# Kernel tuning notes

Hardware: AMD Instinct MI355X
Metric: run time of the kernel (lower is better)

## Reference

```python
import jax, jax.numpy as jnp
import numpy as np

NUM_NODES = 17185
D = 6
FEATS = NUM_NODES * D  # 103110
BATCH = 256
EPS = 1e-5


def setup_inputs() -> dict:
    key = jax.random.key(0)
    ks = jax.random.split(key, 4)
    data = jax.random.normal(ks[0], (BATCH, FEATS), dtype=jnp.float32)
    w_blocks = jax.random.normal(ks[1], (NUM_NODES, D, D), dtype=jnp.float32) * (1.0 / np.sqrt(D))
    b_blocks = jax.random.normal(ks[2], (NUM_NODES, D), dtype=jnp.float32) * 0.1
    fc_w = jax.random.normal(ks[3], (FEATS,), dtype=jnp.float32) * (1.0 / np.sqrt(FEATS))
    return {
        "data": data,
        "w_blocks": w_blocks,
        "b_blocks": b_blocks,
        "bn_gamma": jnp.ones((FEATS,), jnp.float32),
        "bn_beta": jnp.zeros((FEATS,), jnp.float32),
        "bn_mean": jnp.zeros((FEATS,), jnp.float32),
        "bn_var": jnp.ones((FEATS,), jnp.float32),
        "fc_w": fc_w,
        "fc_b": jnp.zeros((1,), jnp.float32),
        "bnf_gamma": jnp.ones((1,), jnp.float32),
        "bnf_beta": jnp.zeros((1,), jnp.float32),
        "bnf_mean": jnp.zeros((1,), jnp.float32),
        "bnf_var": jnp.ones((1,), jnp.float32),
    }


def reference(data, w_blocks, b_blocks, bn_gamma, bn_beta, bn_mean, bn_var,
              fc_w, fc_b, bnf_gamma, bnf_beta, bnf_mean, bnf_var):
    B = data.shape[0]
    # block-diagonal batched matmul replacing 17185 tiny Linear(6,6) calls
    x = data.reshape(B, NUM_NODES, D)                       # [B, N, 6]
    xo = jnp.einsum("bni,noi->bno", x, w_blocks) + b_blocks  # torch Linear: x @ W^T + b
    xo = xo.reshape(B, FEATS)                               # hstack ordering == reshape
    # relu -> BatchNorm1d (eval: running stats) -> dropout (identity in eval)
    h = jnp.maximum(xo, 0.0)
    h = (h - bn_mean) * jax.lax.rsqrt(bn_var + EPS) * bn_gamma + bn_beta
    # final linear [FEATS -> 1], BN(1), sigmoid
    y = h @ fc_w + fc_b                                     # [B]
    y = y[:, None]                                          # [B, 1]
    y = (y - bnf_mean) * jax.lax.rsqrt(bnf_var + EPS) * bnf_gamma + bnf_beta
    return jax.nn.sigmoid(y)
```

## Files before the change

### kernel.cpp

```cpp
#include <hip/hip_runtime.h>
#include <stdint.h>

#define NUM_NODES 17185
#define DD 6
#define FEATS (NUM_NODES * DD)
#define BATCH 256
#define EPS 1e-5f

#define NC 256
#define BC 16
#define NCHUNK ((NUM_NODES + NC - 1) / NC)


__global__ __launch_bounds__(NC) void main_kernel(
    const float* __restrict__ data, const float* __restrict__ wb, const float* __restrict__ bb,
    const float* __restrict__ gamma, const float* __restrict__ var, const float* __restrict__ fcw,
    const float* __restrict__ beta, const float* __restrict__ mean,
    float* __restrict__ pm, float* __restrict__ pc) {

    const int tid = threadIdx.x;
    const int n = blockIdx.x * NC + tid;
    const bool valid = (n < NUM_NODES);

    float wreg[36], bias[6], a[6];
    #pragma unroll
    for (int k = 0; k < 36; k++) wreg[k] = 0.f;
    #pragma unroll
    for (int k = 0; k < 6; k++) { bias[k] = 0.f; a[k] = 0.f; }

    float cnode = 0.f;

    if (valid) {
        const float4* wp = (const float4*)(wb + (size_t)n * 36);
        #pragma unroll
        for (int k = 0; k < 9; k++) {
            float4 v = wp[k];
            wreg[4*k] = v.x; wreg[4*k+1] = v.y; wreg[4*k+2] = v.z; wreg[4*k+3] = v.w;
        }
        const float2* bp = (const float2*)(bb + (size_t)n * 6);
        #pragma unroll
        for (int k = 0; k < 3; k++) { float2 v = bp[k]; bias[2*k] = v.x; bias[2*k+1] = v.y; }
        const int f0 = n * 6;
        const float2* gp = (const float2*)(gamma + f0);
        const float2* vp = (const float2*)(var + f0);
        const float2* fp = (const float2*)(fcw + f0);
        float fw[6];
        #pragma unroll
        for (int k = 0; k < 3; k++) {
            float2 g = gp[k], v = vp[k], f = fp[k];
            fw[2*k] = f.x; fw[2*k+1] = f.y;
            a[2*k]   = g.x * rsqrtf(v.x + EPS) * f.x;
            a[2*k+1] = g.y * rsqrtf(v.y + EPS) * f.y;
        }
        if (blockIdx.y == 0) {
            const float2* bep = (const float2*)(beta + f0);
            const float2* mp  = (const float2*)(mean + f0);
            #pragma unroll
            for (int k = 0; k < 3; k++) {
                float2 be = bep[k], m = mp[k];
                cnode += be.x * fw[2*k]   - m.x * a[2*k];
                cnode += be.y * fw[2*k+1] - m.y * a[2*k+1];
            }
        }
    }

    const int b0 = blockIdx.y * BC;
    float acc[BC];
    #pragma unroll
    for (int r = 0; r < BC; r++) acc[r] = 0.f;

    if (valid) {
        const float2* xbase = (const float2*)(data + (size_t)b0 * FEATS + (size_t)n * 6);
        #pragma unroll
        for (int r = 0; r < BC; r++) {
            const float2* xp = xbase + (size_t)r * (FEATS / 2);
            float2 u0 = xp[0], u1 = xp[1], u2 = xp[2];
            float x0 = u0.x, x1 = u0.y, x2 = u1.x, x3 = u1.y, x4 = u2.x, x5 = u2.y;
            #pragma unroll
            for (int o = 0; o < 6; o++) {
                float s = bias[o];
                s = fmaf(x0, wreg[o*6+0], s);
                s = fmaf(x1, wreg[o*6+1], s);
                s = fmaf(x2, wreg[o*6+2], s);
                s = fmaf(x3, wreg[o*6+3], s);
                s = fmaf(x4, wreg[o*6+4], s);
                s = fmaf(x5, wreg[o*6+5], s);
                acc[r] = fmaf(fmaxf(s, 0.f), a[o], acc[r]);
            }
        }
    }

    __shared__ float red[4][BC];
    #pragma unroll
    for (int r = 0; r < BC; r++) {
        float v = acc[r];
        #pragma unroll
        for (int off = 32; off; off >>= 1) v += __shfl_down(v, off);
        if ((tid & 63) == 0) red[tid >> 6][r] = v;
    }

    if (blockIdx.y == 0) {
        float v = cnode;
        #pragma unroll
        for (int off = 32; off; off >>= 1) v += __shfl_down(v, off);
        __shared__ float credd[4];
        if ((tid & 63) == 0) credd[tid >> 6] = v;
        __syncthreads();
        if (tid == 0) pc[blockIdx.x] = credd[0] + credd[1] + credd[2] + credd[3];
    } else {
        __syncthreads();
    }

    if (tid < BC) {
        float s = red[0][tid] + red[1][tid] + red[2][tid] + red[3][tid];
        pm[blockIdx.x * 256 + b0 + tid] = s;
    }
}

__global__ __launch_bounds__(256) void final_kernel(
    const float* __restrict__ pm, const float* __restrict__ pc,
    const float* __restrict__ fcb, const float* __restrict__ bnfg,
    const float* __restrict__ bnfb, const float* __restrict__ bnfm,
    const float* __restrict__ bnfv, float* __restrict__ out) {
    const int b = threadIdx.x;

    float c = (b < NCHUNK) ? pc[b] : 0.f;
    #pragma unroll
    for (int off = 32; off; off >>= 1) c += __shfl_down(c, off);
    __shared__ float red[4];
    if ((b & 63) == 0) red[b >> 6] = c;
    __syncthreads();
    const float c_sum = red[0] + red[1] + red[2] + red[3];

    float y = 0.f;
    #pragma unroll 4
    for (int ch = 0; ch < NCHUNK; ch++) y += pm[ch * 256 + b];

    y += c_sum + fcb[0];
    float sc = bnfg[0] * rsqrtf(bnfv[0] + EPS);
    float z = (y - bnfm[0]) * sc + bnfb[0];
    out[b] = 1.f / (1.f + expf(-z));
}

extern "C" void kernel_launch(void* const* d_in, const int* in_sizes, int n_in,
                              void* d_out, int out_size, void* d_ws, size_t ws_size,
                              hipStream_t stream) {
    const float* data  = (const float*)d_in[0];
    const float* wb    = (const float*)d_in[1];
    const float* bb    = (const float*)d_in[2];
    const float* gamma = (const float*)d_in[3];
    const float* beta  = (const float*)d_in[4];
    const float* mean  = (const float*)d_in[5];
    const float* var   = (const float*)d_in[6];
    const float* fcw   = (const float*)d_in[7];
    const float* fcb   = (const float*)d_in[8];
    const float* bnfg  = (const float*)d_in[9];
    const float* bnfb  = (const float*)d_in[10];
    const float* bnfm  = (const float*)d_in[11];
    const float* bnfv  = (const float*)d_in[12];

    float* pm = (float*)d_ws;
    float* pc = pm + NCHUNK * 256;

    dim3 grid(NCHUNK, BATCH / BC);
    main_kernel<<<grid, NC, 0, stream>>>(data, wb, bb, gamma, var, fcw, beta, mean, pm, pc);

    final_kernel<<<1, 256, 0, stream>>>(pm, pc, fcb, bnfg, bnfb, bnfm, bnfv, (float*)d_out);
}
```

Before: 191.4 us.

## Stage data rows through shared memory with coalesced float4 loads and register prefetch

Replaces the per-thread strided float2 loads of each node's six features with cooperative, coalesced float4 loads of two batch rows per step into a shared-memory tile. The next pair of rows is prefetched into registers while the current pair is computed. The goal is better global-memory coalescing and overlap of loads with compute. It adds two barriers per step, extra registers and a 12 KB shared buffer, and shared reads at a 24-byte stride per thread may hit bank conflicts.

Measured after the change: 198.7 us. 1.04x slower.

```diff
diff --git a/kernel.cpp b/kernel.cpp
--- a/kernel.cpp
+++ b/kernel.cpp
@@ -10,6 +10,8 @@
 #define NC 256
 #define BC 16
 #define NCHUNK ((NUM_NODES + NC - 1) / NC)
+#define SEG (NC * DD)
+#define TOTF ((size_t)BATCH * FEATS)
 
 
 __global__ __launch_bounds__(NC) void main_kernel(
@@ -21,6 +23,8 @@
     const int tid = threadIdx.x;
     const int n = blockIdx.x * NC + tid;
     const bool valid = (n < NUM_NODES);
+
+    __shared__ float xs[2 * SEG];
 
     float wreg[36], bias[6], a[6];
     #pragma unroll
@@ -65,29 +69,64 @@
     }
 
     const int b0 = blockIdx.y * BC;
+    const size_t segbase = (size_t)blockIdx.x * SEG;
     float acc[BC];
     #pragma unroll
     for (int r = 0; r < BC; r++) acc[r] = 0.f;
 
-    if (valid) {
-        const float2* xbase = (const float2*)(data + (size_t)b0 * FEATS + (size_t)n * 6);
-        #pragma unroll
-        for (int r = 0; r < BC; r++) {
-            const float2* xp = xbase + (size_t)r * (FEATS / 2);
+    float4 pf[3];
+    {
+        #pragma unroll
+        for (int k = 0; k < 3; k++) {
+            int j = tid + k * NC;
+            int row = (j < 384) ? 0 : 1;
+            int col = j - row * 384;
+            size_t g = (size_t)(b0 + row) * FEATS + segbase + (size_t)col * 4;
+            if (g + 4 <= TOTF) pf[k] = *(const float4*)(data + g);
+            else pf[k] = make_float4(0.f, 0.f, 0.f, 0.f);
+        }
+    }
+
+    #pragma unroll
+    for (int s = 0; s < 8; s++) {
+        #pragma unroll
+        for (int k = 0; k < 3; k++) {
+            int j = tid + k * NC;
+            ((float4*)xs)[j] = pf[k];
+        }
+        __syncthreads();
+
+        if (s < 7) {
+            #pragma unroll
+            for (int k = 0; k < 3; k++) {
+                int j = tid + k * NC;
+                int row = (j < 384) ? 0 : 1;
+                int col = j - row * 384;
+                size_t g = (size_t)(b0 + 2*(s+1) + row) * FEATS + segbase + (size_t)col * 4;
+                if (g + 4 <= TOTF) pf[k] = *(const float4*)(data + g);
+                else pf[k] = make_float4(0.f, 0.f, 0.f, 0.f);
+            }
+        }
+
+        #pragma unroll
+        for (int rr = 0; rr < 2; rr++) {
+            const float2* xp = (const float2*)(xs + rr * SEG + tid * 6);
             float2 u0 = xp[0], u1 = xp[1], u2 = xp[2];
             float x0 = u0.x, x1 = u0.y, x2 = u1.x, x3 = u1.y, x4 = u2.x, x5 = u2.y;
+            const int r = 2*s + rr;
             #pragma unroll
             for (int o = 0; o < 6; o++) {
-                float s = bias[o];
-                s = fmaf(x0, wreg[o*6+0], s);
-                s = fmaf(x1, wreg[o*6+1], s);
-                s = fmaf(x2, wreg[o*6+2], s);
-                s = fmaf(x3, wreg[o*6+3], s);
-                s = fmaf(x4, wreg[o*6+4], s);
-                s = fmaf(x5, wreg[o*6+5], s);
-                acc[r] = fmaf(fmaxf(s, 0.f), a[o], acc[r]);
+                float v = bias[o];
+                v = fmaf(x0, wreg[o*6+0], v);
+                v = fmaf(x1, wreg[o*6+1], v);
+                v = fmaf(x2, wreg[o*6+2], v);
+                v = fmaf(x3, wreg[o*6+3], v);
+                v = fmaf(x4, wreg[o*6+4], v);
+                v = fmaf(x5, wreg[o*6+5], v);
+                acc[r] = fmaf(fmaxf(v, 0.f), a[o], acc[r]);
             }
         }
+        __syncthreads();
     }
 
     __shared__ float red[4][BC];
```

## Process two nodes per thread with 16-byte data loads and smaller batch chunks

Applied to the files above, without the earlier changes.

Each thread now handles two adjacent nodes (72 weights in registers), so its 12 contiguous input floats can be read with three 16-byte vector loads instead of three 8-byte loads. Blocks shrink to 128 threads and the batch chunk per block drops from 16 to 8 rows, which doubles the grid along the batch axis and so doubles how many times the weight blocks are re-read. The tail chunk keeps a guarded scalar path. Register pressure rises considerably, and launch bounds now request 4 blocks per CU.

Measured after the change: 261.9 us. +36.8%, slower.

```diff
diff --git a/kernel.cpp b/kernel.cpp
--- a/kernel.cpp
+++ b/kernel.cpp
@@ -1,5 +1,6 @@
 #include <hip/hip_runtime.h>
 #include <stdint.h>
+#include <string.h>
 
 #define NUM_NODES 17185
 #define DD 6
@@ -7,59 +8,73 @@
 #define BATCH 256
 #define EPS 1e-5f
 
-#define NC 256
-#define BC 16
-#define NCHUNK ((NUM_NODES + NC - 1) / NC)
-
-
-__global__ __launch_bounds__(NC) void main_kernel(
+#define NT 128
+#define NPB 256
+#define BC 8
+#define NCHUNK ((NUM_NODES + NPB - 1) / NPB)
+#define TOTF ((size_t)BATCH * FEATS)
+
+
+__device__ __forceinline__ void load16(float* dst, const float* src) {
+    __builtin_memcpy(dst, src, 16);
+}
+
+__global__ __launch_bounds__(NT, 4) void main_kernel(
     const float* __restrict__ data, const float* __restrict__ wb, const float* __restrict__ bb,
     const float* __restrict__ gamma, const float* __restrict__ var, const float* __restrict__ fcw,
     const float* __restrict__ beta, const float* __restrict__ mean,
     float* __restrict__ pm, float* __restrict__ pc) {
 
     const int tid = threadIdx.x;
-    const int n = blockIdx.x * NC + tid;
-    const bool valid = (n < NUM_NODES);
-
-    float wreg[36], bias[6], a[6];
-    #pragma unroll
-    for (int k = 0; k < 36; k++) wreg[k] = 0.f;
-    #pragma unroll
-    for (int k = 0; k < 6; k++) { bias[k] = 0.f; a[k] = 0.f; }
+    const int bx = blockIdx.x;
+    const int n0 = bx * NPB + 2 * tid;
+    const int n1 = n0 + 1;
+    const bool v0 = (n0 < NUM_NODES);
+    const bool v1 = (n1 < NUM_NODES);
+
+    float w[72], bias[12], aa[12];
+    #pragma unroll
+    for (int k = 0; k < 72; k++) w[k] = 0.f;
+    #pragma unroll
+    for (int k = 0; k < 12; k++) { bias[k] = 0.f; aa[k] = 0.f; }
 
     float cnode = 0.f;
 
-    if (valid) {
-        const float4* wp = (const float4*)(wb + (size_t)n * 36);
-        #pragma unroll
-        for (int k = 0; k < 9; k++) {
-            float4 v = wp[k];
-            wreg[4*k] = v.x; wreg[4*k+1] = v.y; wreg[4*k+2] = v.z; wreg[4*k+3] = v.w;
-        }
-        const float2* bp = (const float2*)(bb + (size_t)n * 6);
-        #pragma unroll
-        for (int k = 0; k < 3; k++) { float2 v = bp[k]; bias[2*k] = v.x; bias[2*k+1] = v.y; }
-        const int f0 = n * 6;
-        const float2* gp = (const float2*)(gamma + f0);
-        const float2* vp = (const float2*)(var + f0);
-        const float2* fp = (const float2*)(fcw + f0);
-        float fw[6];
-        #pragma unroll
-        for (int k = 0; k < 3; k++) {
-            float2 g = gp[k], v = vp[k], f = fp[k];
-            fw[2*k] = f.x; fw[2*k+1] = f.y;
-            a[2*k]   = g.x * rsqrtf(v.x + EPS) * f.x;
-            a[2*k+1] = g.y * rsqrtf(v.y + EPS) * f.y;
-        }
-        if (blockIdx.y == 0) {
-            const float2* bep = (const float2*)(beta + f0);
-            const float2* mp  = (const float2*)(mean + f0);
+    #pragma unroll
+    for (int nn = 0; nn < 2; nn++) {
+        const int n = n0 + nn;
+        if (n < NUM_NODES) {
+            const float4* wp = (const float4*)(wb + (size_t)n * 36);
+            #pragma unroll
+            for (int k = 0; k < 9; k++) {
+                float4 v = wp[k];
+                w[nn*36 + 4*k] = v.x; w[nn*36 + 4*k+1] = v.y;
+                w[nn*36 + 4*k+2] = v.z; w[nn*36 + 4*k+3] = v.w;
+            }
+            const float2* bp = (const float2*)(bb + (size_t)n * 6);
+            #pragma unroll
+            for (int k = 0; k < 3; k++) { float2 v = bp[k]; bias[nn*6 + 2*k] = v.x; bias[nn*6 + 2*k+1] = v.y; }
+            const int f0 = n * 6;
+            const float2* gp = (const float2*)(gamma + f0);
+            const float2* vp = (const float2*)(var + f0);
+            const float2* fp = (const float2*)(fcw + f0);
+            float fw[6];
             #pragma unroll
             for (int k = 0; k < 3; k++) {
-                float2 be = bep[k], m = mp[k];
-                cnode += be.x * fw[2*k]   - m.x * a[2*k];
-                cnode += be.y * fw[2*k+1] - m.y * a[2*k+1];
+                float2 g = gp[k], v = vp[k], f = fp[k];
+                fw[2*k] = f.x; fw[2*k+1] = f.y;
+                aa[nn*6 + 2*k]   = g.x * rsqrtf(v.x + EPS) * f.x;
+                aa[nn*6 + 2*k+1] = g.y * rsqrtf(v.y + EPS) * f.y;
+            }
+            if (blockIdx.y == 0) {
+                const float2* bep = (const float2*)(beta + f0);
+                const float2* mp  = (const float2*)(mean + f0);
+                #pragma unroll
+                for (int k = 0; k < 3; k++) {
+                    float2 be = bep[k], m = mp[k];
+                    cnode += be.x * fw[2*k]   - m.x * aa[nn*6 + 2*k];
+                    cnode += be.y * fw[2*k+1] - m.y * aa[nn*6 + 2*k+1];
+                }
             }
         }
     }
@@ -69,28 +84,59 @@
     #pragma unroll
     for (int r = 0; r < BC; r++) acc[r] = 0.f;
 
-    if (valid) {
-        const float2* xbase = (const float2*)(data + (size_t)b0 * FEATS + (size_t)n * 6);
+    if (bx < NCHUNK - 1) {
+        const float* base = data + (size_t)b0 * FEATS + (size_t)bx * (NPB * DD) + 12 * tid;
         #pragma unroll
         for (int r = 0; r < BC; r++) {
-            const float2* xp = xbase + (size_t)r * (FEATS / 2);
-            float2 u0 = xp[0], u1 = xp[1], u2 = xp[2];
-            float x0 = u0.x, x1 = u0.y, x2 = u1.x, x3 = u1.y, x4 = u2.x, x5 = u2.y;
-            #pragma unroll
-            for (int o = 0; o < 6; o++) {
-                float s = bias[o];
-                s = fmaf(x0, wreg[o*6+0], s);
-                s = fmaf(x1, wreg[o*6+1], s);
-                s = fmaf(x2, wreg[o*6+2], s);
-                s = fmaf(x3, wreg[o*6+3], s);
-                s = fmaf(x4, wreg[o*6+4], s);
-                s = fmaf(x5, wreg[o*6+5], s);
-                acc[r] = fmaf(fmaxf(s, 0.f), a[o], acc[r]);
+            const float* p = base + (size_t)r * FEATS;
+            float x[12];
+            load16(x,     p);
+            load16(x + 4, p + 4);
+            load16(x + 8, p + 8);
+            #pragma unroll
+            for (int nn = 0; nn < 2; nn++) {
+                #pragma unroll
+                for (int o = 0; o < 6; o++) {
+                    float s = bias[nn*6 + o];
+                    #pragma unroll
+                    for (int i = 0; i < 6; i++)
+                        s = fmaf(x[nn*6 + i], w[nn*36 + o*6 + i], s);
+                    acc[r] = fmaf(fmaxf(s, 0.f), aa[nn*6 + o], acc[r]);
+                }
             }
         }
-    }
-
-    __shared__ float red[4][BC];
+    } else {
+        #pragma unroll
+        for (int r = 0; r < BC; r++) {
+            const int b = b0 + r;
+            float x[12];
+            #pragma unroll
+            for (int k = 0; k < 12; k++) x[k] = 0.f;
+            if (v0) {
+                const float2* xp = (const float2*)(data + (size_t)b * FEATS + (size_t)n0 * 6);
+                float2 u0 = xp[0], u1 = xp[1], u2 = xp[2];
+                x[0] = u0.x; x[1] = u0.y; x[2] = u1.x; x[3] = u1.y; x[4] = u2.x; x[5] = u2.y;
+            }
+            if (v1) {
+                const float2* xp = (const float2*)(data + (size_t)b * FEATS + (size_t)n1 * 6);
+                float2 u0 = xp[0], u1 = xp[1], u2 = xp[2];
+                x[6] = u0.x; x[7] = u0.y; x[8] = u1.x; x[9] = u1.y; x[10] = u2.x; x[11] = u2.y;
+            }
+            #pragma unroll
+            for (int nn = 0; nn < 2; nn++) {
+                #pragma unroll
+                for (int o = 0; o < 6; o++) {
+                    float s = bias[nn*6 + o];
+                    #pragma unroll
+                    for (int i = 0; i < 6; i++)
+                        s = fmaf(x[nn*6 + i], w[nn*36 + o*6 + i], s);
+                    acc[r] = fmaf(fmaxf(s, 0.f), aa[nn*6 + o], acc[r]);
+                }
+            }
+        }
+    }
+
+    __shared__ float red[2][BC];
     #pragma unroll
     for (int r = 0; r < BC; r++) {
         float v = acc[r];
@@ -103,17 +149,17 @@
         float v = cnode;
         #pragma unroll
         for (int off = 32; off; off >>= 1) v += __shfl_down(v, off);
-        __shared__ float credd[4];
+        __shared__ float credd[2];
         if ((tid & 63) == 0) credd[tid >> 6] = v;
         __syncthreads();
-        if (tid == 0) pc[blockIdx.x] = credd[0] + credd[1] + credd[2] + credd[3];
+        if (tid == 0) pc[bx] = credd[0] + credd[1];
     } else {
         __syncthreads();
     }
 
     if (tid < BC) {
-        float s = red[0][tid] + red[1][tid] + red[2][tid] + red[3][tid];
-        pm[blockIdx.x * 256 + b0 + tid] = s;
+        float s = red[0][tid] + red[1][tid];
+        pm[bx * 256 + b0 + tid] = s;
     }
 }
 
@@ -133,7 +179,7 @@
     const float c_sum = red[0] + red[1] + red[2] + red[3];
 
     float y = 0.f;
-    #pragma unroll 4
+    #pragma unroll 8
     for (int ch = 0; ch < NCHUNK; ch++) y += pm[ch * 256 + b];
 
     y += c_sum + fcb[0];
@@ -163,7 +209,7 @@
     float* pc = pm + NCHUNK * 256;
 
     dim3 grid(NCHUNK, BATCH / BC);
-    main_kernel<<<grid, NC, 0, stream>>>(data, wb, bb, gamma, var, fcw, beta, mean, pm, pc);
+    main_kernel<<<grid, NT, 0, stream>>>(data, wb, bb, gamma, var, fcw, beta, mean, pm, pc);
 
     final_kernel<<<1, 256, 0, stream>>>(pm, pc, fcb, bnfg, bnfb, bnfm, bnfv, (float*)d_out);
 }
```

## Fuse final reduction via last-block atomic counter; nontemporal double-buffered data loads

Applied to the files above, without the earlier changes.

Removes the separate final_kernel launch: each block increments a global counter after a threadfence, and the last block to finish does the cross-chunk reduction and sigmoid. The per-row data loads become nontemporal 64-bit loads, issued four rows at a time with a double buffer so the next group is in flight while the current one is computed. This cuts a kernel launch and tail gap and should improve memory-level parallelism, but it adds a memset launch, an atomic per block and higher register pressure.

Result: slower. 362.7 us (+89.4%).

```diff
diff --git a/kernel.cpp b/kernel.cpp
--- a/kernel.cpp
+++ b/kernel.cpp
@@ -10,16 +10,28 @@
 #define NC 256
 #define BC 16
 #define NCHUNK ((NUM_NODES + NC - 1) / NC)
-
+#define NBLK (NCHUNK * (BATCH / BC))
+
+
+__device__ __forceinline__ void nt_load2(const float* p, float& lo, float& hi) {
+    uint64_t u = __builtin_nontemporal_load((const uint64_t*)p);
+    lo = __uint_as_float((uint32_t)u);
+    hi = __uint_as_float((uint32_t)(u >> 32));
+}
 
 __global__ __launch_bounds__(NC) void main_kernel(
     const float* __restrict__ data, const float* __restrict__ wb, const float* __restrict__ bb,
     const float* __restrict__ gamma, const float* __restrict__ var, const float* __restrict__ fcw,
     const float* __restrict__ beta, const float* __restrict__ mean,
-    float* __restrict__ pm, float* __restrict__ pc) {
+    const float* __restrict__ fcb, const float* __restrict__ bnfg,
+    const float* __restrict__ bnfb, const float* __restrict__ bnfm,
+    const float* __restrict__ bnfv,
+    float* __restrict__ pm, float* __restrict__ pc, unsigned int* __restrict__ ctr,
+    float* __restrict__ out) {
 
     const int tid = threadIdx.x;
-    const int n = blockIdx.x * NC + tid;
+    const int bx = blockIdx.x;
+    const int n = bx * NC + tid;
     const bool valid = (n < NUM_NODES);
 
     float wreg[36], bias[6], a[6];
@@ -70,22 +82,41 @@
     for (int r = 0; r < BC; r++) acc[r] = 0.f;
 
     if (valid) {
-        const float2* xbase = (const float2*)(data + (size_t)b0 * FEATS + (size_t)n * 6);
-        #pragma unroll
-        for (int r = 0; r < BC; r++) {
-            const float2* xp = xbase + (size_t)r * (FEATS / 2);
-            float2 u0 = xp[0], u1 = xp[1], u2 = xp[2];
-            float x0 = u0.x, x1 = u0.y, x2 = u1.x, x3 = u1.y, x4 = u2.x, x5 = u2.y;
+        const float* xb = data + (size_t)b0 * FEATS + (size_t)n * 6;
+        float xr[2][4][6];
+        #pragma unroll
+        for (int j = 0; j < 4; j++) {
+            const float* p = xb + (size_t)j * FEATS;
+            nt_load2(p,     xr[0][j][0], xr[0][j][1]);
+            nt_load2(p + 2, xr[0][j][2], xr[0][j][3]);
+            nt_load2(p + 4, xr[0][j][4], xr[0][j][5]);
+        }
+        #pragma unroll
+        for (int g = 0; g < 4; g++) {
+            const int cur = g & 1;
+            if (g < 3) {
+                #pragma unroll
+                for (int j = 0; j < 4; j++) {
+                    const float* p = xb + (size_t)((g + 1) * 4 + j) * FEATS;
+                    nt_load2(p,     xr[cur ^ 1][j][0], xr[cur ^ 1][j][1]);
+                    nt_load2(p + 2, xr[cur ^ 1][j][2], xr[cur ^ 1][j][3]);
+                    nt_load2(p + 4, xr[cur ^ 1][j][4], xr[cur ^ 1][j][5]);
+                }
+            }
             #pragma unroll
-            for (int o = 0; o < 6; o++) {
-                float s = bias[o];
-                s = fmaf(x0, wreg[o*6+0], s);
-                s = fmaf(x1, wreg[o*6+1], s);
-                s = fmaf(x2, wreg[o*6+2], s);
-                s = fmaf(x3, wreg[o*6+3], s);
-                s = fmaf(x4, wreg[o*6+4], s);
-                s = fmaf(x5, wreg[o*6+5], s);
-                acc[r] = fmaf(fmaxf(s, 0.f), a[o], acc[r]);
+            for (int j = 0; j < 4; j++) {
+                const int r = 4 * g + j;
+                #pragma unroll
+                for (int o = 0; o < 6; o++) {
+                    float s = bias[o];
+                    s = fmaf(xr[cur][j][0], wreg[o*6+0], s);
+                    s = fmaf(xr[cur][j][1], wreg[o*6+1], s);
+                    s = fmaf(xr[cur][j][2], wreg[o*6+2], s);
+                    s = fmaf(xr[cur][j][3], wreg[o*6+3], s);
+                    s = fmaf(xr[cur][j][4], wreg[o*6+4], s);
+                    s = fmaf(xr[cur][j][5], wreg[o*6+5], s);
+                    acc[r] = fmaf(fmaxf(s, 0.f), a[o], acc[r]);
+                }
             }
         }
     }
@@ -99,47 +130,51 @@
         if ((tid & 63) == 0) red[tid >> 6][r] = v;
     }
 
+    __shared__ float credd[4];
     if (blockIdx.y == 0) {
         float v = cnode;
         #pragma unroll
         for (int off = 32; off; off >>= 1) v += __shfl_down(v, off);
-        __shared__ float credd[4];
         if ((tid & 63) == 0) credd[tid >> 6] = v;
-        __syncthreads();
-        if (tid == 0) pc[blockIdx.x] = credd[0] + credd[1] + credd[2] + credd[3];
-    } else {
-        __syncthreads();
-    }
+    }
+    __syncthreads();
 
     if (tid < BC) {
         float s = red[0][tid] + red[1][tid] + red[2][tid] + red[3][tid];
-        pm[blockIdx.x * 256 + b0 + tid] = s;
-    }
-}
-
-__global__ __launch_bounds__(256) void final_kernel(
-    const float* __restrict__ pm, const float* __restrict__ pc,
-    const float* __restrict__ fcb, const float* __restrict__ bnfg,
-    const float* __restrict__ bnfb, const float* __restrict__ bnfm,
-    const float* __restrict__ bnfv, float* __restrict__ out) {
-    const int b = threadIdx.x;
-
-    float c = (b < NCHUNK) ? pc[b] : 0.f;
-    #pragma unroll
-    for (int off = 32; off; off >>= 1) c += __shfl_down(c, off);
-    __shared__ float red[4];
-    if ((b & 63) == 0) red[b >> 6] = c;
+        pm[bx * 256 + b0 + tid] = s;
+    }
+    if (blockIdx.y == 0 && tid == 0) {
+        pc[bx] = credd[0] + credd[1] + credd[2] + credd[3];
+    }
+
+    __threadfence();
     __syncthreads();
-    const float c_sum = red[0] + red[1] + red[2] + red[3];
-
-    float y = 0.f;
-    #pragma unroll 4
-    for (int ch = 0; ch < NCHUNK; ch++) y += pm[ch * 256 + b];
-
-    y += c_sum + fcb[0];
-    float sc = bnfg[0] * rsqrtf(bnfv[0] + EPS);
-    float z = (y - bnfm[0]) * sc + bnfb[0];
-    out[b] = 1.f / (1.f + expf(-z));
+    __shared__ unsigned int islast;
+    if (tid == 0) {
+        unsigned int old = atomicAdd(ctr, 1u);
+        islast = (old == NBLK - 1) ? 1u : 0u;
+    }
+    __syncthreads();
+    if (islast) {
+        __threadfence();
+        const int b = tid;
+        float c = (b < NCHUNK) ? pc[b] : 0.f;
+        #pragma unroll
+        for (int off = 32; off; off >>= 1) c += __shfl_down(c, off);
+        __shared__ float cred[4];
+        if ((b & 63) == 0) cred[b >> 6] = c;
+        __syncthreads();
+        const float c_sum = cred[0] + cred[1] + cred[2] + cred[3];
+
+        float y = 0.f;
+        #pragma unroll 4
+        for (int ch = 0; ch < NCHUNK; ch++) y += pm[ch * 256 + b];
+
+        y += c_sum + fcb[0];
+        const float sc = bnfg[0] * rsqrtf(bnfv[0] + EPS);
+        const float z = (y - bnfm[0]) * sc + bnfb[0];
+        out[b] = 1.f / (1.f + expf(-z));
+    }
 }
 
 extern "C" void kernel_launch(void* const* d_in, const int* in_sizes, int n_in,
@@ -161,9 +196,12 @@
 
     float* pm = (float*)d_ws;
     float* pc = pm + NCHUNK * 256;
+    unsigned int* ctr = (unsigned int*)(pc + NCHUNK);
+
+    (void)hipMemsetAsync(ctr, 0, sizeof(unsigned int), stream);
 
     dim3 grid(NCHUNK, BATCH / BC);
-    main_kernel<<<grid, NC, 0, stream>>>(data, wb, bb, gamma, var, fcw, beta, mean, pm, pc);
-
-    final_kernel<<<1, 256, 0, stream>>>(pm, pc, fcb, bnfg, bnfb, bnfm, bnfv, (float*)d_out);
+    main_kernel<<<grid, NC, 0, stream>>>(data, wb, bb, gamma, var, fcw, beta, mean,
+                                         fcb, bnfg, bnfb, bnfm, bnfv,
+                                         pm, pc, ctr, (float*)d_out);
 }
```
